# Kernel tuning notes

Hardware: AMD Instinct MI355X
Metric: run time of the kernel (lower is better)

## Reference

```python
import jax, jax.numpy as jnp
import numpy as np

N = 8192      # total nodes
BG = 8        # graphs in batch
NPG = 1024    # nodes per graph
DEG = 8       # in-degree per node
E = N * DEG   # edges
Q = 16        # queries per graph
D = 768       # in_dim
H = 4         # heads
F = 768       # h_feats per head
HD = H * F    # 3072


def setup_inputs() -> dict:
    key = jax.random.key(0)
    ks = jax.random.split(key, 24)
    x = jax.random.normal(ks[0], (N, D), jnp.float32)
    # block-diagonal random graph: every node has DEG incoming edges from its own graph
    edge_dst = jnp.repeat(jnp.arange(N), DEG)
    edge_src = (edge_dst // NPG) * NPG + jax.random.randint(ks[1], (E,), 0, NPG)
    query_embedding = jax.random.normal(ks[2], (BG, Q, D), jnp.float32) * 0.02
    bert_score = jax.random.uniform(ks[3], (BG, Q, NPG), jnp.float32)

    def lin(k, i, o):
        return jax.random.normal(k, (i, o), jnp.float32) * (1.0 / np.sqrt(i))

    inp = dict(x=x, edge_src=edge_src, edge_dst=edge_dst,
               query_embedding=query_embedding, bert_score=bert_score)
    inp['W1'] = lin(ks[4], D, HD)
    inp['attn_l1'] = jax.random.normal(ks[5], (H, F), jnp.float32) * 0.1
    inp['attn_r1'] = jax.random.normal(ks[6], (H, F), jnp.float32) * 0.1
    inp['b1'] = jax.random.normal(ks[7], (HD,), jnp.float32) * 0.02
    inp['gamma1'] = 1.0 + 0.1 * jax.random.normal(ks[8], (HD,), jnp.float32)
    inp['beta1'] = 0.1 * jax.random.normal(ks[9], (HD,), jnp.float32)
    inp['prelu1'] = 0.25 + 0.01 * jax.random.normal(ks[10], (HD,), jnp.float32)
    inp['W2'] = lin(ks[11], HD, HD)
    inp['attn_l2'] = jax.random.normal(ks[12], (H, F), jnp.float32) * 0.1
    inp['attn_r2'] = jax.random.normal(ks[13], (H, F), jnp.float32) * 0.1
    inp['b2'] = jax.random.normal(ks[14], (HD,), jnp.float32) * 0.02
    inp['gamma2'] = 1.0 + 0.1 * jax.random.normal(ks[15], (HD,), jnp.float32)
    inp['beta2'] = 0.1 * jax.random.normal(ks[16], (HD,), jnp.float32)
    inp['prelu2'] = 0.25 + 0.01 * jax.random.normal(ks[17], (HD,), jnp.float32)
    return inp


def _gat_layer(h, src, dst, W, al, ar, b, gamma, beta, pa):
    # DGL GATConv (eval mode, no residual): fc -> edge attention -> segment softmax -> scatter-sum
    feat = (h @ W).reshape(N, H, F)
    el = jnp.einsum('nhf,hf->nh', feat, al)            # [N,H]
    er = jnp.einsum('nhf,hf->nh', feat, ar)
    e = el[src] + er[dst]                              # [E,H]
    e = jnp.where(e > 0, e, 0.2 * e)                   # leaky_relu(0.2)
    m = jax.ops.segment_max(e, dst, num_segments=N)
    a = jnp.exp(e - m[dst])
    denom = jax.ops.segment_sum(a, dst, num_segments=N)
    alpha = a / denom[dst]                             # edge softmax over in-edges
    rst = jax.ops.segment_sum(feat[src] * alpha[:, :, None], dst, num_segments=N)
    hflat = (rst + b.reshape(1, H, F)).reshape(N, HD)
    # BatchNorm1d (training-mode batch statistics, biased var)
    mu = hflat.mean(axis=0)
    var = hflat.var(axis=0)
    hn = (hflat - mu) * jax.lax.rsqrt(var + 1e-5) * gamma + beta
    # PReLU (per-channel)
    return jnp.where(hn > 0, hn, pa * hn)


def _lambda_mrr(y_pred, y_true):
    # y_pred/y_true: [Q,K]; no padding in this pipeline (y_true = 1/rank > 0)
    order = jnp.argsort(-y_pred, axis=-1)
    yp = jnp.take_along_axis(y_pred, order, axis=-1)
    yt = jnp.take_along_axis(y_true, order, axis=-1)
    mask = (yt[:, :, None] - yt[:, None, :] > 0).astype(yp.dtype)
    sdiff = jnp.clip(yp[:, :, None] - yp[:, None, :], -50.0, 50.0)
    losses = jnp.log1p(jnp.exp(-sdiff))
    return (losses * mask).sum() / mask.sum()


def _forward(x, edge_src, edge_dst, query_embedding, bert_score,
             W1, attn_l1, attn_r1, b1, gamma1, beta1, prelu1,
             W2, attn_l2, attn_r2, b2, gamma2, beta2, prelu2):
    h1 = _gat_layer(x, edge_src, edge_dst, W1, attn_l1, attn_r1, b1, gamma1, beta1, prelu1)
    m1 = h1.reshape(N, H, F).mean(axis=1)
    h2 = _gat_layer(h1, edge_src, edge_dst, W2, attn_l2, attn_r2, b2, gamma2, beta2, prelu2)
    m2 = h2.reshape(N, H, F).mean(axis=1)
    node_rep = jnp.maximum(m1, m2)                      # JumpingKnowledge(max)

    reps = node_rep.reshape(BG, NPG, F)                 # per-graph reps
    reps_flat = node_rep                                # [N,F]
    graph_of = jnp.repeat(jnp.arange(BG), NPG)          # [N]
    rank_gt = (1.0 / jnp.arange(1, NPG + 1, dtype=jnp.float32))[None, :]  # [1,K]

    def per_graph(i, rep_i, q, bs):
        order = jnp.argsort(-bs, axis=-1)               # [Q,NPG] bert rank (desc)
        p = rep_i[order[:, 0]]                          # [Q,F] positive
        neg = rep_i[order[:, 1:]]                       # [Q,NPG-1,F] own negatives
        p_sim = jnp.sum(q * p, axis=-1, keepdims=True)  # [Q,1]
        own_sim = jnp.einsum('qf,qkf->qk', q, neg)      # [Q,NPG-1]
        all_sim = q @ reps_flat.T                       # [Q,N] for in-batch negatives
        other = (graph_of != i).astype(q.dtype)         # mask out own graph
        rank_pred = jnp.concatenate([p_sim, own_sim], axis=-1)  # first K cols of ranking_list
        mrr = _lambda_mrr(rank_pred, jnp.broadcast_to(rank_gt, rank_pred.shape))
        pe = jnp.exp(p_sim).sum(axis=-1)
        ne = jnp.exp(own_sim).sum(axis=-1) + (jnp.exp(all_sim) * other).sum(axis=-1)
        cl = jnp.mean(-jnp.log(pe / (pe + ne)))
        logp = jax.nn.log_softmax(q @ rep_i.T, axis=-1)
        ent = jnp.mean(-(jnp.exp(logp) * logp).sum(axis=-1))
        return cl, mrr, ent

    cl_g, mrr_g, ent_g = jax.vmap(per_graph)(jnp.arange(BG), reps, query_embedding, bert_score)
    return cl_g.mean(), mrr_g.mean(), ent_g.mean()


def reference(x, edge_src, edge_dst, query_embedding, bert_score,
              W1, attn_l1, attn_r1, b1, gamma1, beta1, prelu1,
              W2, attn_l2, attn_r2, b2, gamma2, beta2, prelu2):
    return _forward(x, edge_src, edge_dst, query_embedding, bert_score,
                    W1, attn_l1, attn_r1, b1, gamma1, beta1, prelu1,
                    W2, attn_l2, attn_r2, b2, gamma2, beta2, prelu2)
```

## Files before the change

kernel.cpp:

```cpp
#include <hip/hip_runtime.h>
#include <hip/hip_bf16.h>
#include <hip/hip_fp16.h>

#define NN 8192
#define DD 768
#define HH 4
#define FF 768
#define HD 3072
#define BGr 8
#define NPGr 1024
#define QQ 16
#define NQ 128
#define DEGr 8
#define MRR_TILES 36
#define WSCALE 32.0f
#define WSCALE_INV 0.03125f

typedef __attribute__((ext_vector_type(8))) short bf16x8;
typedef __attribute__((ext_vector_type(4))) float f32x4;
typedef __attribute__((ext_vector_type(4))) int i32x4;
typedef __attribute__((ext_vector_type(8))) int i32x8;

__device__ __forceinline__ unsigned short f2bf(float f) {
    union { float f; unsigned u; } v; v.f = f;
    unsigned u = v.u;
    unsigned r = (u + 0x7fffu + ((u >> 16) & 1u)) >> 16;
    return (unsigned short)r;
}
__device__ __forceinline__ float bf2f(unsigned short u) {
    union { unsigned u; float f; } v; v.u = ((unsigned)u) << 16;
    return v.f;
}
__device__ __forceinline__ unsigned char f2fp8(float x) {
    unsigned s = (__float_as_uint(x) >> 24) & 0x80;
    __half h = __float2half(fabsf(x) * 0.00390625f);
    unsigned t = (unsigned)__half_as_ushort(h);
    t += 0x3F + ((t >> 7) & 1);
    unsigned b = t >> 7;
    if (b > 0x7E) b = 0x7E;
    return (unsigned char)(s | b);
}
__device__ __forceinline__ float fp82f(unsigned u) {
    unsigned short hb = (unsigned short)(((u & 0x80) << 8) | ((u & 0x7F) << 7));
    return __half2float(__ushort_as_half(hb)) * 256.f;
}

__device__ __forceinline__ void gl_lds16(const void* g, void* l) {
    __builtin_amdgcn_global_load_lds(
        (const __attribute__((address_space(1))) unsigned int*)g,
        (__attribute__((address_space(3))) unsigned int*)l, 16, 0, 0);
}

#define PB_Z 13
#define PB_CX (PB_Z + 6144)
#define PB_CQ (PB_CX + 96)
#define PB_T1 (PB_CQ + 2304)
#define PB_T2 (PB_T1 + 9216)
__global__ __launch_bounds__(256) void prep_k(const float* __restrict__ x,
                                              unsigned char* __restrict__ xb,
                                              const float* __restrict__ qe,
                                              unsigned short* __restrict__ qeb,
                                              const float* __restrict__ W1,
                                              unsigned char* __restrict__ w1t,
                                              const float* __restrict__ W2,
                                              unsigned char* __restrict__ w2t,
                                              float* __restrict__ stats1,
                                              float* __restrict__ stats2,
                                              float* __restrict__ out) {
    __shared__ float tile[32][33];
    int blk = blockIdx.x, tid = threadIdx.x;
    if (blk < PB_Z) {
        int f = blk * 1024 + tid * 4;
        if (f < 2 * HD) *(float4*)&stats1[f] = make_float4(0.f, 0.f, 0.f, 0.f);
        else if (f < 4 * HD) *(float4*)&stats2[f - 2 * HD] = make_float4(0.f, 0.f, 0.f, 0.f);
        else if (f == 4 * HD) { out[0] = 0.f; out[1] = 0.f; out[2] = 0.f; }
    } else if (blk < PB_CX) {
        int i = (blk - PB_Z) * 256 + tid;
        float4 v = ((const float4*)x)[i];
        uchar4 o;
        o.x = f2fp8(v.x); o.y = f2fp8(v.y); o.z = f2fp8(v.z); o.w = f2fp8(v.w);
        ((uchar4*)xb)[i] = o;
    } else if (blk < PB_CQ) {
        int i = (blk - PB_CX) * 256 + tid;
        float4 v = ((const float4*)qe)[i];
        ushort4 o;
        o.x = f2bf(v.x); o.y = f2bf(v.y); o.z = f2bf(v.z); o.w = f2bf(v.w);
        ((ushort4*)qeb)[i] = o;
    } else {
        const float* in; unsigned char* outp; int K, t;
        if (blk < PB_T1) { in = W1; outp = w1t; K = DD; t = blk - PB_CQ; }
        else             { in = W2; outp = w2t; K = HD; t = blk - PB_T1; }
        int n0 = (t % 96) * 32, k0 = (t / 96) * 32;
        int tx = tid & 31, ty = tid >> 5;
        #pragma unroll
        for (int i = 0; i < 4; i++) {
            int r = ty + i * 8;
            tile[r][tx] = in[(size_t)(k0 + r) * HD + n0 + tx];
        }
        __syncthreads();
        #pragma unroll
        for (int i = 0; i < 4; i++) {
            int r = ty + i * 8;
            outp[(size_t)(n0 + r) * K + k0 + tx] = f2fp8(tile[tx][r] * WSCALE);
        }
    }
}

template <bool EPI>
__global__ __launch_bounds__(256) void gemm_fp8(const unsigned char* __restrict__ A,
                                                const unsigned char* __restrict__ BT,
                                                unsigned char* __restrict__ C,
                                                float* __restrict__ elp,
                                                float* __restrict__ erp,
                                                const float* __restrict__ al,
                                                const float* __restrict__ ar,
                                                int M, int Nc, int K, float inv_scale) {
    __shared__ __align__(16) unsigned char As[2][128 * 128];
    __shared__ __align__(16) unsigned char Bs[2][128 * 128];
    int tid = threadIdx.x;
    int m0 = blockIdx.x * 128;
    int n0 = blockIdx.y * 128;
    int w = tid >> 6, lane = tid & 63;
    int wr = w >> 1, wc = w & 1;
    int lm = lane & 15, lq = lane >> 4;

    f32x4 acc[4][4] = {};

    int srow = tid >> 3, su = tid & 7;
    const unsigned char* Ag0[4];
    const unsigned char* Bg0[4];
    unsigned char* AsW[2][4];
    unsigned char* BsW[2][4];
    #pragma unroll
    for (int s = 0; s < 4; s++) {
        int row = srow + 32 * s;
        int uu = su ^ (row & 7);
        Ag0[s] = A  + (size_t)(m0 + row) * K + uu * 16;
        Bg0[s] = BT + (size_t)(n0 + row) * K + uu * 16;
        #pragma unroll
        for (int b = 0; b < 2; b++) {
            AsW[b][s] = &As[b][row * 128 + su * 16];
            BsW[b][s] = &Bs[b][row * 128 + su * 16];
        }
    }

    int NT = K >> 7;
    #pragma unroll
    for (int s = 0; s < 4; s++) {
        gl_lds16(Ag0[s], AsW[0][s]);
        gl_lds16(Bg0[s], BsW[0][s]);
    }

    for (int kt = 0; kt < NT; ++kt) {
        int cur = kt & 1;
        if (kt + 1 < NT) {
            int kb = (kt + 1) << 7;
            #pragma unroll
            for (int s = 0; s < 4; s++) {
                gl_lds16(Ag0[s] + kb, AsW[cur ^ 1][s]);
                gl_lds16(Bg0[s] + kb, BsW[cur ^ 1][s]);
            }
            asm volatile("s_waitcnt vmcnt(8)" ::: "memory");
        } else {
            asm volatile("s_waitcnt vmcnt(0)" ::: "memory");
        }
        asm volatile("s_barrier" ::: "memory");

        const unsigned char* Ab = &As[cur][0];
        const unsigned char* Bb = &Bs[cur][0];
        i32x8 af[4];
        #pragma unroll
        for (int i = 0; i < 4; i++) {
            int row = wr * 64 + i * 16 + lm;
            int sw = (row & 7) << 4;
            i32x4 lo = *(const i32x4*)&Ab[row * 128 + ((lq * 32) ^ sw)];
            i32x4 hi = *(const i32x4*)&Ab[row * 128 + ((lq * 32 + 16) ^ sw)];
            i32x8 v;
            v[0] = lo[0]; v[1] = lo[1]; v[2] = lo[2]; v[3] = lo[3];
            v[4] = hi[0]; v[5] = hi[1]; v[6] = hi[2]; v[7] = hi[3];
            af[i] = v;
        }
        #pragma unroll
        for (int j = 0; j < 4; j++) {
            int row = wc * 64 + j * 16 + lm;
            int sw = (row & 7) << 4;
            i32x4 lo = *(const i32x4*)&Bb[row * 128 + ((lq * 32) ^ sw)];
            i32x4 hi = *(const i32x4*)&Bb[row * 128 + ((lq * 32 + 16) ^ sw)];
            i32x8 bv;
            bv[0] = lo[0]; bv[1] = lo[1]; bv[2] = lo[2]; bv[3] = lo[3];
            bv[4] = hi[0]; bv[5] = hi[1]; bv[6] = hi[2]; bv[7] = hi[3];
            #pragma unroll
            for (int i = 0; i < 4; i++)
                acc[i][j] = __builtin_amdgcn_mfma_scale_f32_16x16x128_f8f6f4(
                    af[i], bv, acc[i][j], 0, 0, 0, 127, 0, 127);
        }
        asm volatile("s_barrier" ::: "memory");
    }

    #pragma unroll
    for (int i = 0; i < 4; i++)
        #pragma unroll
        for (int j = 0; j < 4; j++)
            #pragma unroll
            for (int r = 0; r < 4; r++)
                acc[i][j][r] *= inv_scale;

    #pragma unroll
    for (int i = 0; i < 4; i++) {
        int row = m0 + wr * 64 + i * 16 + lq * 4;
        #pragma unroll
        for (int j = 0; j < 4; j++) {
            int col = n0 + wc * 64 + j * 16 + lm;
            #pragma unroll
            for (int r = 0; r < 4; r++)
                C[(size_t)(row + r) * Nc + col] = f2fp8(acc[i][j][r]);
        }
    }

    if (EPI) {
        int h = n0 / FF;
        int cb = (n0 % FF) >> 7;
        float alv[4], arv[4];
        #pragma unroll
        for (int j = 0; j < 4; j++) {
            int col = n0 + wc * 64 + j * 16 + lm;
            alv[j] = al[col];
            arv[j] = ar[col];
        }
        #pragma unroll
        for (int i = 0; i < 4; i++) {
            #pragma unroll
            for (int r = 0; r < 4; r++) {
                float se = acc[i][0][r] * alv[0] + acc[i][1][r] * alv[1]
                         + acc[i][2][r] * alv[2] + acc[i][3][r] * alv[3];
                float sr_ = acc[i][0][r] * arv[0] + acc[i][1][r] * arv[1]
                          + acc[i][2][r] * arv[2] + acc[i][3][r] * arv[3];
                #pragma unroll
                for (int mm = 1; mm <= 8; mm <<= 1) {
                    se  += __shfl_xor(se, mm, 64);
                    sr_ += __shfl_xor(sr_, mm, 64);
                }
                if (lm == 0) {
                    int row = m0 + wr * 64 + i * 16 + lq * 4 + r;
                    size_t slot = ((size_t)row * HH + h) * 12 + cb * 2 + wc;
                    elp[slot] = se;
                    erp[slot] = sr_;
                }
            }
        }
    }
}

__global__ __launch_bounds__(256) void gemm_bt(const unsigned short* __restrict__ A,
                                               const unsigned short* __restrict__ BT,
                                               float* __restrict__ Ct,
                                               int M, int Nc, int K) {
    __shared__ unsigned short As[128 * 64];
    __shared__ unsigned short Bs[128 * 64];
    int tid = threadIdx.x;
    int m0 = blockIdx.x * 128;
    int n0 = blockIdx.y * 128;
    int w = tid >> 6, lane = tid & 63;
    int wr = w >> 1, wc = w & 1;
    int lm = lane & 15, lq = lane >> 4;

    f32x4 acc[4][4] = {};

    int pc = tid & 7;
    const unsigned short* Ag[4];
    const unsigned short* Bg[4];
    unsigned short* AsW[4];
    unsigned short* BsW[4];
    #pragma unroll
    for (int s = 0; s < 4; s++) {
        int row = (tid >> 3) + 32 * s;
        int lc = pc ^ (row & 7);
        Ag[s]  = A  + (size_t)(m0 + row) * K + lc * 8;
        Bg[s]  = BT + (size_t)(n0 + row) * K + lc * 8;
        AsW[s] = &As[(row * 8 + pc) * 8];
        BsW[s] = &Bs[(row * 8 + pc) * 8];
    }

    for (int k0 = 0; k0 < K; k0 += 64) {
        __syncthreads();
        #pragma unroll
        for (int s = 0; s < 4; s++) {
            gl_lds16(Ag[s], AsW[s]);
            gl_lds16(Bg[s], BsW[s]);
        }
        __syncthreads();

        #pragma unroll
        for (int kk = 0; kk < 2; kk++) {
            bf16x8 af[4], bfr[4];
            #pragma unroll
            for (int i = 0; i < 4; i++) {
                int row = wr * 64 + i * 16 + lm;
                int phys = (kk * 4 + lq) ^ (row & 7);
                af[i] = *(const bf16x8*)&As[row * 64 + phys * 8];
            }
            #pragma unroll
            for (int j = 0; j < 4; j++) {
                int row = wc * 64 + j * 16 + lm;
                int phys = (kk * 4 + lq) ^ (row & 7);
                bfr[j] = *(const bf16x8*)&Bs[row * 64 + phys * 8];
            }
            #pragma unroll
            for (int i = 0; i < 4; i++)
                #pragma unroll
                for (int j = 0; j < 4; j++)
                    acc[i][j] = __builtin_amdgcn_mfma_f32_16x16x32_bf16(af[i], bfr[j], acc[i][j], 0, 0, 0);
        }

        #pragma unroll
        for (int s = 0; s < 4; s++) { Ag[s] += 64; Bg[s] += 64; }
    }

    #pragma unroll
    for (int i = 0; i < 4; i++) {
        int row = m0 + wr * 64 + i * 16 + lq * 4;
        #pragma unroll
        for (int j = 0; j < 4; j++) {
            int col = n0 + wc * 64 + j * 16 + lm;
            float4 o = make_float4(acc[i][j][0], acc[i][j][1], acc[i][j][2], acc[i][j][3]);
            *(float4*)&Ct[(size_t)col * M + row] = o;
        }
    }
}

__global__ __launch_bounds__(384) void aggregate_k(const unsigned char* __restrict__ feat,
                                                   const float* __restrict__ elp,
                                                   const float* __restrict__ erp,
                                                   const int* __restrict__ esrc,
                                                   const float* __restrict__ bias,
                                                   unsigned short* __restrict__ out) {
    int b = blockIdx.x;
    int nbase = (b & 7) * NPGr + (b >> 3) * 8;
    int t = threadIdx.x;
    __shared__ int s_src[8][DEGr];
    __shared__ float s_el[8][DEGr][HH];
    __shared__ float s_er[8][HH];
    __shared__ float s_alpha[8][DEGr][HH];
    if (t < 64) s_src[t >> 3][t & 7] = esrc[(size_t)(nbase + (t >> 3)) * DEGr + (t & 7)];
    __syncthreads();
    if (t < 256) {
        int nd = t >> 5, k = (t >> 2) & 7, h = t & 3;
        const float* pp = &elp[((size_t)s_src[nd][k] * HH + h) * 12];
        float s = 0.f;
        #pragma unroll
        for (int q = 0; q < 12; q++) s += pp[q];
        s_el[nd][k][h] = s;
    }
    if (t < 32) {
        int nd = t >> 2, h = t & 3;
        const float* pp = &erp[((size_t)(nbase + nd) * HH + h) * 12];
        float s = 0.f;
        #pragma unroll
        for (int q = 0; q < 12; q++) s += pp[q];
        s_er[nd][h] = s;
    }
    __syncthreads();
    if (t < 32) {
        int nd = t >> 2, h = t & 3;
        float e[DEGr], m = -1e30f;
        #pragma unroll
        for (int k = 0; k < DEGr; k++) {
            float v = s_el[nd][k][h] + s_er[nd][h];
            v = v > 0.f ? v : 0.2f * v;
            e[k] = v; m = fmaxf(m, v);
        }
        float d = 0.f;
        #pragma unroll
        for (int k = 0; k < DEGr; k++) { e[k] = __expf(e[k] - m); d += e[k]; }
        float inv = 1.0f / d;
        #pragma unroll
        for (int k = 0; k < DEGr; k++) s_alpha[nd][k][h] = e[k] * inv;
    }
    __syncthreads();

    int c8 = t * 8;
    int h = t / 96;
    float4 b0 = *(const float4*)&bias[c8];
    float4 b1 = *(const float4*)&bias[c8 + 4];
    float bb[8] = {b0.x, b0.y, b0.z, b0.w, b1.x, b1.y, b1.z, b1.w};
    #pragma unroll
    for (int nd = 0; nd < 8; nd++) {
        float a[8] = {bb[0], bb[1], bb[2], bb[3], bb[4], bb[5], bb[6], bb[7]};
        #pragma unroll
        for (int k = 0; k < DEGr; k++) {
            float wv = s_alpha[nd][k][h];
            unsigned long fv = *(const unsigned long*)&feat[(size_t)s_src[nd][k] * HD + c8];
            #pragma unroll
            for (int e = 0; e < 8; e++)
                a[e] += wv * fp82f((unsigned)((fv >> (8 * e)) & 0xFF));
        }
        union { unsigned short u[8]; bf16x8 v; } o;
        #pragma unroll
        for (int e = 0; e < 8; e++) o.u[e] = f2bf(a[e]);
        *(bf16x8*)&out[(size_t)(nbase + nd) * HD + c8] = o.v;
    }
}

__global__ __launch_bounds__(256) void ln_stats_k(const unsigned short* __restrict__ x,
                                                  float* __restrict__ sums) {
    int col = (blockIdx.x * 256 + threadIdx.x) * 4;
    int r0 = blockIdx.y * 128;
    float s[4] = {0.f, 0.f, 0.f, 0.f}, s2[4] = {0.f, 0.f, 0.f, 0.f};
    for (int r = r0; r < r0 + 128; r++) {
        ushort4 v = *(const ushort4*)&x[(size_t)r * HD + col];
        float f0 = bf2f(v.x), f1 = bf2f(v.y), f2 = bf2f(v.z), f3 = bf2f(v.w);
        s[0] += f0; s[1] += f1; s[2] += f2; s[3] += f3;
        s2[0] += f0 * f0; s2[1] += f1 * f1; s2[2] += f2 * f2; s2[3] += f3 * f3;
    }
    #pragma unroll
    for (int e = 0; e < 4; e++) {
        atomicAdd(&sums[col + e], s[e]);
        atomicAdd(&sums[HD + col + e], s2[e]);
    }
}

__device__ __forceinline__ void ln_vals(const unsigned short* __restrict__ x, int n, int col,
                                        const float* __restrict__ sums,
                                        const float* __restrict__ gamma,
                                        const float* __restrict__ beta,
                                        const float* __restrict__ prelu,
                                        float* val) {
    const float invN = 1.0f / (float)NN;
    ushort4 v = *(const ushort4*)&x[(size_t)n * HD + col];
    float4 sm = *(const float4*)&sums[col];
    float4 sq = *(const float4*)&sums[HD + col];
    float4 g = *(const float4*)&gamma[col];
    float4 b = *(const float4*)&beta[col];
    float4 p = *(const float4*)&prelu[col];
    float vv[4] = {bf2f(v.x), bf2f(v.y), bf2f(v.z), bf2f(v.w)};
    float ss[4] = {sm.x, sm.y, sm.z, sm.w};
    float qq[4] = {sq.x, sq.y, sq.z, sq.w};
    float gg[4] = {g.x, g.y, g.z, g.w};
    float bb[4] = {b.x, b.y, b.z, b.w};
    float pp[4] = {p.x, p.y, p.z, p.w};
    #pragma unroll
    for (int e = 0; e < 4; e++) {
        float mu = ss[e] * invN;
        float var = qq[e] * invN - mu * mu;
        float rs = rsqrtf(var + 1e-5f);
        float t = (vv[e] - mu) * rs * gg[e] + bb[e];
        val[e] = t > 0.f ? t : pp[e] * t;
    }
}

__global__ __launch_bounds__(192) void ln_norm_mean_k(const unsigned short* __restrict__ x,
                                                      const float* __restrict__ sums,
                                                      const float* __restrict__ gamma,
                                                      const float* __restrict__ beta,
                                                      const float* __restrict__ prelu,
                                                      unsigned char* __restrict__ h,
                                                      unsigned short* __restrict__ m1) {
    int n = blockIdx.x, tid = threadIdx.x;
    int c = tid * 4;
    float acc4[4] = {0.f, 0.f, 0.f, 0.f};
    #pragma unroll
    for (int hh = 0; hh < HH; hh++) {
        int col = hh * FF + c;
        float val[4];
        ln_vals(x, n, col, sums, gamma, beta, prelu, val);
        uchar4 o;
        o.x = f2fp8(val[0]); o.y = f2fp8(val[1]); o.z = f2fp8(val[2]); o.w = f2fp8(val[3]);
        *(uchar4*)&h[(size_t)n * HD + col] = o;
        #pragma unroll
        for (int e = 0; e < 4; e++) acc4[e] += val[e];
    }
    ushort4 o;
    o.x = f2bf(0.25f * acc4[0]); o.y = f2bf(0.25f * acc4[1]);
    o.z = f2bf(0.25f * acc4[2]); o.w = f2bf(0.25f * acc4[3]);
    *(ushort4*)&m1[(size_t)n * FF + c] = o;
}

__global__ __launch_bounds__(192) void ln_norm_rep_k(const unsigned short* __restrict__ x,
                                                     const float* __restrict__ sums,
                                                     const float* __restrict__ gamma,
                                                     const float* __restrict__ beta,
                                                     const float* __restrict__ prelu,
                                                     const unsigned short* __restrict__ m1,
                                                     unsigned short* __restrict__ rep) {
    int n = blockIdx.x, tid = threadIdx.x;
    int c = tid * 4;
    float acc4[4] = {0.f, 0.f, 0.f, 0.f};
    #pragma unroll
    for (int hh = 0; hh < HH; hh++) {
        int col = hh * FF + c;
        float val[4];
        ln_vals(x, n, col, sums, gamma, beta, prelu, val);
        #pragma unroll
        for (int e = 0; e < 4; e++) acc4[e] += val[e];
    }
    ushort4 m = *(const ushort4*)&m1[(size_t)n * FF + c];
    ushort4 o;
    o.x = f2bf(fmaxf(bf2f(m.x), 0.25f * acc4[0]));
    o.y = f2bf(fmaxf(bf2f(m.y), 0.25f * acc4[1]));
    o.z = f2bf(fmaxf(bf2f(m.z), 0.25f * acc4[2]));
    o.w = f2bf(fmaxf(bf2f(m.w), 0.25f * acc4[3]));
    *(ushort4*)&rep[(size_t)n * FF + c] = o;
}

__global__ __launch_bounds__(256) void loss_k(const float* __restrict__ simsQ,
                                              const float* __restrict__ bert,
                                              float* __restrict__ out) {
    __shared__ float s_ya[128];
    __shared__ float s_ba[128];
    __shared__ float red[256];
    __shared__ int redi[256];
    int tid = threadIdx.x;

    if (blockIdx.x < NQ * MRR_TILES) {
        int qq = blockIdx.x / MRR_TILES;
        int t36 = blockIdx.x % MRR_TILES;
        int I = 0, rem = t36;
        while (rem >= 8 - I) { rem -= 8 - I; I++; }
        int J = I + rem;
        int g = qq >> 4;
        const float* Y = simsQ + (size_t)qq * NN + (size_t)g * NPGr;
        const float* B = bert + (size_t)qq * NPGr;
        int a0 = I * 128, b0 = J * 128;

        if (tid < 128) s_ya[tid] = Y[a0 + tid];
        else           s_ba[tid - 128] = B[a0 + (tid - 128)];
        int bl = tid & 127;
        int bcol = b0 + bl;
        float yb = Y[bcol];
        float bbv = B[bcol];
        __syncthreads();

        const float L2E = 1.44269504f;
        int abase = (tid >> 7) * 64;
        float s = 0.f;
        if (I == J) {
            #pragma unroll 4
            for (int ai = 0; ai < 64; ai++) {
                int a = abase + ai;
                float ya = s_ya[a], ba = s_ba[a];
                float tdf = ya - yb;
                float d = (bbv > ba) ? tdf : -tdf;
                float xv = fminf(fmaxf(d, -50.f), 50.f);
                float term = __builtin_amdgcn_logf(1.0f + __builtin_amdgcn_exp2f(xv * L2E));
                s += (bl > a) ? term : 0.f;
            }
        } else {
            #pragma unroll 4
            for (int ai = 0; ai < 64; ai++) {
                int a = abase + ai;
                float ya = s_ya[a], ba = s_ba[a];
                float tdf = ya - yb;
                float d = (bbv > ba) ? tdf : -tdf;
                float xv = fminf(fmaxf(d, -50.f), 50.f);
                s += __builtin_amdgcn_logf(1.0f + __builtin_amdgcn_exp2f(xv * L2E));
            }
        }
        red[tid] = s; __syncthreads();
        for (int o = 128; o; o >>= 1) { if (tid < o) red[tid] += red[tid + o]; __syncthreads(); }
        if (tid == 0)
            atomicAdd(&out[1], red[0] * (0.69314718f / (523776.0f * (float)NQ)));
    } else {
        int qq = blockIdx.x - NQ * MRR_TILES;
        int g = qq >> 4;
        const float* S = simsQ + (size_t)qq * NN;
        const float* Sg = S + g * NPGr;
        float m = -1e30f;
        for (int n = tid; n < NN; n += 256) m = fmaxf(m, S[n]);
        red[tid] = m; __syncthreads();
        for (int o = 128; o; o >>= 1) { if (tid < o) red[tid] = fmaxf(red[tid], red[tid + o]); __syncthreads(); }
        float mAll = red[0]; __syncthreads();
        float mg = -1e30f;
        for (int j = tid; j < NPGr; j += 256) mg = fmaxf(mg, Sg[j]);
        red[tid] = mg; __syncthreads();
        for (int o = 128; o; o >>= 1) { if (tid < o) red[tid] = fmaxf(red[tid], red[tid + o]); __syncthreads(); }
        float mG = red[0]; __syncthreads();
        float z = 0.f;
        for (int n = tid; n < NN; n += 256) z += __expf(S[n] - mAll);
        red[tid] = z; __syncthreads();
        for (int o = 128; o; o >>= 1) { if (tid < o) red[tid] += red[tid + o]; __syncthreads(); }
        float Zall = red[0]; __syncthreads();
        float zg = 0.f, tg = 0.f;
        for (int j = tid; j < NPGr; j += 256) {
            float s = Sg[j];
            float e = __expf(s - mG);
            zg += e; tg += e * s;
        }
        red[tid] = zg; __syncthreads();
        for (int o = 128; o; o >>= 1) { if (tid < o) red[tid] += red[tid + o]; __syncthreads(); }
        float Zg = red[0]; __syncthreads();
        red[tid] = tg; __syncthreads();
        for (int o = 128; o; o >>= 1) { if (tid < o) red[tid] += red[tid + o]; __syncthreads(); }
        float Tg = red[0]; __syncthreads();
        float bb = -1e30f; int bi = NPGr;
        for (int j = tid; j < NPGr; j += 256) {
            float v = bert[(size_t)qq * NPGr + j];
            if (v > bb) { bb = v; bi = j; }
        }
        red[tid] = bb; redi[tid] = bi; __syncthreads();
        for (int o = 128; o; o >>= 1) {
            if (tid < o) {
                if (red[tid + o] > red[tid] || (red[tid + o] == red[tid] && redi[tid + o] < redi[tid])) {
                    red[tid] = red[tid + o]; redi[tid] = redi[tid + o];
                }
            }
            __syncthreads();
        }
        if (tid == 0) {
            float p_sim = Sg[redi[0]];
            float lse = mAll + logf(Zall);
            atomicAdd(&out[0], (lse - p_sim) * (1.0f / (float)NQ));
            float entv = (mG + logf(Zg)) - Tg / Zg;
            atomicAdd(&out[2], entv * (1.0f / (float)NQ));
        }
    }
}

extern "C" void kernel_launch(void* const* d_in, const int* in_sizes, int n_in,
                              void* d_out, int out_size, void* d_ws, size_t ws_size,
                              hipStream_t stream) {
    const float* x    = (const float*)d_in[0];
    const int* esrc   = (const int*)d_in[1];
    const float* qe   = (const float*)d_in[3];
    const float* bert = (const float*)d_in[4];
    const float* W1   = (const float*)d_in[5];
    const float* al1  = (const float*)d_in[6];
    const float* ar1  = (const float*)d_in[7];
    const float* b1   = (const float*)d_in[8];
    const float* g1   = (const float*)d_in[9];
    const float* be1  = (const float*)d_in[10];
    const float* p1   = (const float*)d_in[11];
    const float* W2   = (const float*)d_in[12];
    const float* al2  = (const float*)d_in[13];
    const float* ar2  = (const float*)d_in[14];
    const float* b2   = (const float*)d_in[15];
    const float* g2   = (const float*)d_in[16];
    const float* be2  = (const float*)d_in[17];
    const float* p2   = (const float*)d_in[18];
    float* out = (float*)d_out;
    (void)in_sizes; (void)n_in; (void)out_size; (void)ws_size;

    char* p = (char*)d_ws;
    auto alloc = [&](size_t bytes) -> void* {
        void* r = (void*)p;
        p += (bytes + 255) & ~(size_t)255;
        return r;
    };
    unsigned char*  featB = (unsigned char*)alloc((size_t)NN * HD);
    unsigned short* hflat = (unsigned short*)alloc((size_t)NN * HD * 2);
    unsigned char*  hbuf  = (unsigned char*)alloc((size_t)NN * HD);
    unsigned short* repb  = (unsigned short*)alloc((size_t)NN * FF * 2);
    unsigned char*  w1t   = (unsigned char*)alloc((size_t)HD * DD);
    unsigned char*  w2t   = (unsigned char*)alloc((size_t)HD * HD);
    unsigned short* m1    = (unsigned short*)alloc((size_t)NN * FF * 2);
    float* elp            = (float*)alloc((size_t)NN * HH * 12 * 4);
    float* erp            = (float*)alloc((size_t)NN * HH * 12 * 4);
    unsigned short* qeb   = (unsigned short*)alloc((size_t)NQ * FF * 2);
    float* simsQ          = (float*)alloc((size_t)NQ * NN * 4);
    float* stats1         = (float*)alloc((size_t)2 * HD * 4);
    float* stats2         = (float*)alloc((size_t)2 * HD * 4);
    unsigned char* xb     = (unsigned char*)repb;

    prep_k<<<PB_T2, 256, 0, stream>>>(x, xb, qe, qeb, W1, w1t, W2, w2t, stats1, stats2, out);

    gemm_fp8<true><<<dim3(NN / 128, HD / 128), 256, 0, stream>>>(
        xb, w1t, featB, elp, erp, al1, ar1, NN, HD, DD, WSCALE_INV);
    aggregate_k<<<NN / 8, 384, 0, stream>>>(featB, elp, erp, esrc, b1, hflat);
    ln_stats_k<<<dim3(HD / 1024, NN / 128), 256, 0, stream>>>(hflat, stats1);
    ln_norm_mean_k<<<NN, 192, 0, stream>>>(hflat, stats1, g1, be1, p1, hbuf, m1);

    gemm_fp8<true><<<dim3(NN / 128, HD / 128), 256, 0, stream>>>(
        hbuf, w2t, featB, elp, erp, al2, ar2, NN, HD, HD, WSCALE_INV);
    aggregate_k<<<NN / 8, 384, 0, stream>>>(featB, elp, erp, esrc, b2, hflat);
    ln_stats_k<<<dim3(HD / 1024, NN / 128), 256, 0, stream>>>(hflat, stats2);
    ln_norm_rep_k<<<NN, 192, 0, stream>>>(hflat, stats2, g2, be2, p2, m1, repb);

    gemm_bt<<<dim3(NN / 128, 1), 256, 0, stream>>>(repb, qeb, simsQ, NN, NQ, FF);

    loss_k<<<NQ * MRR_TILES + NQ, 256, 0, stream>>>(simsQ, bert, out);
}
```

Measured before the change: 545.4 us.

## Use hardware FP8 conversions, raise MFMA priority, batch LN rows per block

Replaces the software FP8 encode/decode with the gfx950 packed cvt builtins, where available, in prep, the GEMM epilogue, aggregation and LN output. It also wraps the MFMA loop in s_setprio so the math waves get issue priority. The LN normalize kernels now handle 8 rows per block and hoist the per-column mean, scale, beta and prelu values into registers, cutting the block count and the repeated stats loads. The hardware conversion may round or saturate differently from the manual e4m3 emulation, which includes a 1/256 scaling, so numerics could shift.

```diff
diff --git a/kernel.cpp b/kernel.cpp
--- a/kernel.cpp
+++ b/kernel.cpp
@@ -18,8 +18,15 @@
 
 typedef __attribute__((ext_vector_type(8))) short bf16x8;
 typedef __attribute__((ext_vector_type(4))) float f32x4;
+typedef __attribute__((ext_vector_type(2))) float f32x2;
 typedef __attribute__((ext_vector_type(4))) int i32x4;
 typedef __attribute__((ext_vector_type(8))) int i32x8;
+
+#if defined(__has_builtin)
+#  if __has_builtin(__builtin_amdgcn_cvt_pk_fp8_f32) && __has_builtin(__builtin_amdgcn_cvt_pk_f32_fp8)
+#    define HW_FP8 1
+#  endif
+#endif
 
 __device__ __forceinline__ unsigned short f2bf(float f) {
     union { float f; unsigned u; } v; v.f = f;
@@ -43,6 +50,23 @@
 __device__ __forceinline__ float fp82f(unsigned u) {
     unsigned short hb = (unsigned short)(((u & 0x80) << 8) | ((u & 0x7F) << 7));
     return __half2float(__ushort_as_half(hb)) * 256.f;
+}
+__device__ __forceinline__ unsigned char f2fp8_s(float x) {
+#ifdef HW_FP8
+    return (unsigned char)(__builtin_amdgcn_cvt_pk_fp8_f32(x, x, 0, false) & 0xFF);
+#else
+    return f2fp8(x);
+#endif
+}
+__device__ __forceinline__ unsigned f2fp8x4(float a, float b, float c, float d) {
+#ifdef HW_FP8
+    int lo = __builtin_amdgcn_cvt_pk_fp8_f32(a, b, 0, false);
+    int full = __builtin_amdgcn_cvt_pk_fp8_f32(c, d, lo, true);
+    return (unsigned)full;
+#else
+    return (unsigned)f2fp8(a) | ((unsigned)f2fp8(b) << 8) |
+           ((unsigned)f2fp8(c) << 16) | ((unsigned)f2fp8(d) << 24);
+#endif
 }
 
 __device__ __forceinline__ void gl_lds16(const void* g, void* l) {
@@ -77,9 +101,7 @@
     } else if (blk < PB_CX) {
         int i = (blk - PB_Z) * 256 + tid;
         float4 v = ((const float4*)x)[i];
-        uchar4 o;
-        o.x = f2fp8(v.x); o.y = f2fp8(v.y); o.z = f2fp8(v.z); o.w = f2fp8(v.w);
-        ((uchar4*)xb)[i] = o;
+        ((unsigned*)xb)[i] = f2fp8x4(v.x, v.y, v.z, v.w);
     } else if (blk < PB_CQ) {
         int i = (blk - PB_CX) * 256 + tid;
         float4 v = ((const float4*)qe)[i];
@@ -101,7 +123,7 @@
         #pragma unroll
         for (int i = 0; i < 4; i++) {
             int r = ty + i * 8;
-            outp[(size_t)(n0 + r) * K + k0 + tx] = f2fp8(tile[tx][r] * WSCALE);
+            outp[(size_t)(n0 + r) * K + k0 + tx] = f2fp8_s(tile[tx][r] * WSCALE);
         }
     }
 }
@@ -180,6 +202,7 @@
             v[4] = hi[0]; v[5] = hi[1]; v[6] = hi[2]; v[7] = hi[3];
             af[i] = v;
         }
+        __builtin_amdgcn_s_setprio(1);
         #pragma unroll
         for (int j = 0; j < 4; j++) {
             int row = wc * 64 + j * 16 + lm;
@@ -194,6 +217,7 @@
                 acc[i][j] = __builtin_amdgcn_mfma_scale_f32_16x16x128_f8f6f4(
                     af[i], bv, acc[i][j], 0, 0, 0, 127, 0, 127);
         }
+        __builtin_amdgcn_s_setprio(0);
         asm volatile("s_barrier" ::: "memory");
     }
 
@@ -213,7 +237,7 @@
             int col = n0 + wc * 64 + j * 16 + lm;
             #pragma unroll
             for (int r = 0; r < 4; r++)
-                C[(size_t)(row + r) * Nc + col] = f2fp8(acc[i][j][r]);
+                C[(size_t)(row + r) * Nc + col] = f2fp8_s(acc[i][j][r]);
         }
     }
 
@@ -390,9 +414,21 @@
         for (int k = 0; k < DEGr; k++) {
             float wv = s_alpha[nd][k][h];
             unsigned long fv = *(const unsigned long*)&feat[(size_t)s_src[nd][k] * HD + c8];
+#ifdef HW_FP8
+            unsigned w0 = (unsigned)fv, w1 = (unsigned)(fv >> 32);
+            f32x2 d0 = __builtin_amdgcn_cvt_pk_f32_fp8((int)w0, false);
+            f32x2 d1 = __builtin_amdgcn_cvt_pk_f32_fp8((int)w0, true);
+            f32x2 d2 = __builtin_amdgcn_cvt_pk_f32_fp8((int)w1, false);
+            f32x2 d3 = __builtin_amdgcn_cvt_pk_f32_fp8((int)w1, true);
+            a[0] += wv * d0[0]; a[1] += wv * d0[1];
+            a[2] += wv * d1[0]; a[3] += wv * d1[1];
+            a[4] += wv * d2[0]; a[5] += wv * d2[1];
+            a[6] += wv * d3[0]; a[7] += wv * d3[1];
+#else
             #pragma unroll
             for (int e = 0; e < 8; e++)
                 a[e] += wv * fp82f((unsigned)((fv >> (8 * e)) & 0xFF));
+#endif
         }
         union { unsigned short u[8]; bf16x8 v; } o;
         #pragma unroll
@@ -419,35 +455,6 @@
     }
 }
 
-__device__ __forceinline__ void ln_vals(const unsigned short* __restrict__ x, int n, int col,
-                                        const float* __restrict__ sums,
-                                        const float* __restrict__ gamma,
-                                        const float* __restrict__ beta,
-                                        const float* __restrict__ prelu,
-                                        float* val) {
-    const float invN = 1.0f / (float)NN;
-    ushort4 v = *(const ushort4*)&x[(size_t)n * HD + col];
-    float4 sm = *(const float4*)&sums[col];
-    float4 sq = *(const float4*)&sums[HD + col];
-    float4 g = *(const float4*)&gamma[col];
-    float4 b = *(const float4*)&beta[col];
-    float4 p = *(const float4*)&prelu[col];
-    float vv[4] = {bf2f(v.x), bf2f(v.y), bf2f(v.z), bf2f(v.w)};
-    float ss[4] = {sm.x, sm.y, sm.z, sm.w};
-    float qq[4] = {sq.x, sq.y, sq.z, sq.w};
-    float gg[4] = {g.x, g.y, g.z, g.w};
-    float bb[4] = {b.x, b.y, b.z, b.w};
-    float pp[4] = {p.x, p.y, p.z, p.w};
-    #pragma unroll
-    for (int e = 0; e < 4; e++) {
-        float mu = ss[e] * invN;
-        float var = qq[e] * invN - mu * mu;
-        float rs = rsqrtf(var + 1e-5f);
-        float t = (vv[e] - mu) * rs * gg[e] + bb[e];
-        val[e] = t > 0.f ? t : pp[e] * t;
-    }
-}
-
 __global__ __launch_bounds__(192) void ln_norm_mean_k(const unsigned short* __restrict__ x,
                                                       const float* __restrict__ sums,
                                                       const float* __restrict__ gamma,
@@ -455,24 +462,52 @@
                                                       const float* __restrict__ prelu,
                                                       unsigned char* __restrict__ h,
                                                       unsigned short* __restrict__ m1) {
-    int n = blockIdx.x, tid = threadIdx.x;
+    int n0 = blockIdx.x * 8, tid = threadIdx.x;
     int c = tid * 4;
-    float acc4[4] = {0.f, 0.f, 0.f, 0.f};
+    const float invN = 1.0f / (float)NN;
+    float mu_[HH][4], aa_[HH][4], bb_[HH][4], pp_[HH][4];
     #pragma unroll
     for (int hh = 0; hh < HH; hh++) {
         int col = hh * FF + c;
-        float val[4];
-        ln_vals(x, n, col, sums, gamma, beta, prelu, val);
-        uchar4 o;
-        o.x = f2fp8(val[0]); o.y = f2fp8(val[1]); o.z = f2fp8(val[2]); o.w = f2fp8(val[3]);
-        *(uchar4*)&h[(size_t)n * HD + col] = o;
-        #pragma unroll
-        for (int e = 0; e < 4; e++) acc4[e] += val[e];
-    }
-    ushort4 o;
-    o.x = f2bf(0.25f * acc4[0]); o.y = f2bf(0.25f * acc4[1]);
-    o.z = f2bf(0.25f * acc4[2]); o.w = f2bf(0.25f * acc4[3]);
-    *(ushort4*)&m1[(size_t)n * FF + c] = o;
+        float4 sm = *(const float4*)&sums[col];
+        float4 sq = *(const float4*)&sums[HD + col];
+        float4 g = *(const float4*)&gamma[col];
+        float4 b = *(const float4*)&beta[col];
+        float4 p = *(const float4*)&prelu[col];
+        float smv[4] = {sm.x, sm.y, sm.z, sm.w}, sqv[4] = {sq.x, sq.y, sq.z, sq.w};
+        float gv[4] = {g.x, g.y, g.z, g.w}, bv[4] = {b.x, b.y, b.z, b.w};
+        float pv[4] = {p.x, p.y, p.z, p.w};
+        #pragma unroll
+        for (int e = 0; e < 4; e++) {
+            float mu = smv[e] * invN;
+            float var = sqv[e] * invN - mu * mu;
+            float rs = rsqrtf(var + 1e-5f);
+            mu_[hh][e] = mu; aa_[hh][e] = rs * gv[e];
+            bb_[hh][e] = bv[e]; pp_[hh][e] = pv[e];
+        }
+    }
+    for (int nd = 0; nd < 8; nd++) {
+        int n = n0 + nd;
+        float acc4[4] = {0.f, 0.f, 0.f, 0.f};
+        #pragma unroll
+        for (int hh = 0; hh < HH; hh++) {
+            int col = hh * FF + c;
+            ushort4 v = *(const ushort4*)&x[(size_t)n * HD + col];
+            float vv[4] = {bf2f(v.x), bf2f(v.y), bf2f(v.z), bf2f(v.w)};
+            float val[4];
+            #pragma unroll
+            for (int e = 0; e < 4; e++) {
+                float t = (vv[e] - mu_[hh][e]) * aa_[hh][e] + bb_[hh][e];
+                val[e] = t > 0.f ? t : pp_[hh][e] * t;
+                acc4[e] += val[e];
+            }
+            *(unsigned*)&h[(size_t)n * HD + col] = f2fp8x4(val[0], val[1], val[2], val[3]);
+        }
+        ushort4 o;
+        o.x = f2bf(0.25f * acc4[0]); o.y = f2bf(0.25f * acc4[1]);
+        o.z = f2bf(0.25f * acc4[2]); o.w = f2bf(0.25f * acc4[3]);
+        *(ushort4*)&m1[(size_t)n * FF + c] = o;
+    }
 }
 
 __global__ __launch_bounds__(192) void ln_norm_rep_k(const unsigned short* __restrict__ x,
@@ -482,24 +517,52 @@
                                                      const float* __restrict__ prelu,
                                                      const unsigned short* __restrict__ m1,
                                                      unsigned short* __restrict__ rep) {
-    int n = blockIdx.x, tid = threadIdx.x;
+    int n0 = blockIdx.x * 8, tid = threadIdx.x;
     int c = tid * 4;
-    float acc4[4] = {0.f, 0.f, 0.f, 0.f};
+    const float invN = 1.0f / (float)NN;
+    float mu_[HH][4], aa_[HH][4], bb_[HH][4], pp_[HH][4];
     #pragma unroll
     for (int hh = 0; hh < HH; hh++) {
         int col = hh * FF + c;
-        float val[4];
-        ln_vals(x, n, col, sums, gamma, beta, prelu, val);
-        #pragma unroll
-        for (int e = 0; e < 4; e++) acc4[e] += val[e];
-    }
-    ushort4 m = *(const ushort4*)&m1[(size_t)n * FF + c];
-    ushort4 o;
-    o.x = f2bf(fmaxf(bf2f(m.x), 0.25f * acc4[0]));
-    o.y = f2bf(fmaxf(bf2f(m.y), 0.25f * acc4[1]));
-    o.z = f2bf(fmaxf(bf2f(m.z), 0.25f * acc4[2]));
-    o.w = f2bf(fmaxf(bf2f(m.w), 0.25f * acc4[3]));
-    *(ushort4*)&rep[(size_t)n * FF + c] = o;
+        float4 sm = *(const float4*)&sums[col];
+        float4 sq = *(const float4*)&sums[HD + col];
+        float4 g = *(const float4*)&gamma[col];
+        float4 b = *(const float4*)&beta[col];
+        float4 p = *(const float4*)&prelu[col];
+        float smv[4] = {sm.x, sm.y, sm.z, sm.w}, sqv[4] = {sq.x, sq.y, sq.z, sq.w};
+        float gv[4] = {g.x, g.y, g.z, g.w}, bv[4] = {b.x, b.y, b.z, b.w};
+        float pv[4] = {p.x, p.y, p.z, p.w};
+        #pragma unroll
+        for (int e = 0; e < 4; e++) {
+            float mu = smv[e] * invN;
+            float var = sqv[e] * invN - mu * mu;
+            float rs = rsqrtf(var + 1e-5f);
+            mu_[hh][e] = mu; aa_[hh][e] = rs * gv[e];
+            bb_[hh][e] = bv[e]; pp_[hh][e] = pv[e];
+        }
+    }
+    for (int nd = 0; nd < 8; nd++) {
+        int n = n0 + nd;
+        float acc4[4] = {0.f, 0.f, 0.f, 0.f};
+        #pragma unroll
+        for (int hh = 0; hh < HH; hh++) {
+            int col = hh * FF + c;
+            ushort4 v = *(const ushort4*)&x[(size_t)n * HD + col];
+            float vv[4] = {bf2f(v.x), bf2f(v.y), bf2f(v.z), bf2f(v.w)};
+            #pragma unroll
+            for (int e = 0; e < 4; e++) {
+                float t = (vv[e] - mu_[hh][e]) * aa_[hh][e] + bb_[hh][e];
+                acc4[e] += t > 0.f ? t : pp_[hh][e] * t;
+            }
+        }
+        ushort4 m = *(const ushort4*)&m1[(size_t)n * FF + c];
+        ushort4 o;
+        o.x = f2bf(fmaxf(bf2f(m.x), 0.25f * acc4[0]));
+        o.y = f2bf(fmaxf(bf2f(m.y), 0.25f * acc4[1]));
+        o.z = f2bf(fmaxf(bf2f(m.z), 0.25f * acc4[2]));
+        o.w = f2bf(fmaxf(bf2f(m.w), 0.25f * acc4[3]));
+        *(ushort4*)&rep[(size_t)n * FF + c] = o;
+    }
 }
 
 __global__ __launch_bounds__(256) void loss_k(const float* __restrict__ simsQ,
@@ -666,13 +729,13 @@
         xb, w1t, featB, elp, erp, al1, ar1, NN, HD, DD, WSCALE_INV);
     aggregate_k<<<NN / 8, 384, 0, stream>>>(featB, elp, erp, esrc, b1, hflat);
     ln_stats_k<<<dim3(HD / 1024, NN / 128), 256, 0, stream>>>(hflat, stats1);
-    ln_norm_mean_k<<<NN, 192, 0, stream>>>(hflat, stats1, g1, be1, p1, hbuf, m1);
+    ln_norm_mean_k<<<NN / 8, 192, 0, stream>>>(hflat, stats1, g1, be1, p1, hbuf, m1);
 
     gemm_fp8<true><<<dim3(NN / 128, HD / 128), 256, 0, stream>>>(
         hbuf, w2t, featB, elp, erp, al2, ar2, NN, HD, HD, WSCALE_INV);
     aggregate_k<<<NN / 8, 384, 0, stream>>>(featB, elp, erp, esrc, b2, hflat);
     ln_stats_k<<<dim3(HD / 1024, NN / 128), 256, 0, stream>>>(hflat, stats2);
-    ln_norm_rep_k<<<NN, 192, 0, stream>>>(hflat, stats2, g2, be2, p2, m1, repb);
+    ln_norm_rep_k<<<NN / 8, 192, 0, stream>>>(hflat, stats2, g2, be2, p2, m1, repb);
 
     gemm_bt<<<dim3(NN / 128, 1), 256, 0, stream>>>(repb, qeb, simsQ, NN, NQ, FF);
 
```

New measurement: 489.3 us, median of 2. 10.3% less time.
